# Kernel optimization log

Hardware: AMD Instinct MI355X
Metric: run time of the kernel (lower is better)

Reference implementation:

```python
import jax, jax.numpy as jnp
import numpy as np

IMG = 640.0  # pixel coordinate range for keypoints


def setup_inputs() -> dict:
    key = jax.random.key(0)
    ks = jax.random.split(key, 16)
    B, N, M, C, D, G = 4, 4096, 4096, 256, 256, 32
    s = 1.0 / np.sqrt(C)
    inp = {
        "nodes_t": jax.random.normal(ks[0], (B, N, C), jnp.float32),
        "nodes_t1": jax.random.normal(ks[1], (B, M, C), jnp.float32),
        "kpts_t1_pred": jax.random.uniform(ks[2], (B, N, 2), jnp.float32) * IMG,
        "kpts_t1_actual": jax.random.uniform(ks[3], (B, M, 2), jnp.float32) * IMG,
        "Wq": jax.random.normal(ks[4], (D, C), jnp.float32) * s,
        "bq": jnp.zeros((D,), jnp.float32),
        "Wk": jax.random.normal(ks[5], (D, C), jnp.float32) * s,
        "bk": jnp.zeros((D,), jnp.float32),
        "Wv": jax.random.normal(ks[6], (D, C), jnp.float32) * s,
        "bv": jnp.zeros((D,), jnp.float32),
        "Wm": jax.random.normal(ks[7], (D, D), jnp.float32) * (1.0 / np.sqrt(D)),
        "bm": jnp.zeros((D,), jnp.float32),
        "Wg1": jax.random.normal(ks[8], (G, 3), jnp.float32) * (1.0 / np.sqrt(3.0)),
        "bg1": jnp.zeros((G,), jnp.float32),
        "Wg2": jax.random.normal(ks[9], (G, G), jnp.float32) * (1.0 / np.sqrt(G)),
        "bg2": jnp.zeros((G,), jnp.float32),
        "iter_idx": 0,
    }
    return inp


def reference(nodes_t, nodes_t1, kpts_t1_pred, kpts_t1_actual,
              Wq, bq, Wk, bk, Wv, bv, Wm, bm, Wg1, bg1, Wg2, bg2, iter_idx):
    # window size schedule (iter_idx is a static Python int)
    win = 64.0 if iter_idx == 0 else max(4.0, 32.0 / 2 ** (iter_idx - 1))

    Q = nodes_t @ Wq.T + bq      # [B,N,256]
    K = nodes_t1 @ Wk.T + bk     # [B,M,256]
    V = nodes_t1 @ Wv.T + bv     # [B,M,256]

    # distance-based window mask [B,N,M]
    du = jnp.abs(kpts_t1_pred[:, :, 0:1] - kpts_t1_actual[:, None, :, 0])
    dv = jnp.abs(kpts_t1_pred[:, :, 1:2] - kpts_t1_actual[:, None, :, 1])
    mask = (du < win) & (dv < win)

    attn = jnp.einsum('bnd,bmd->bnm', Q, K) / jnp.sqrt(jnp.float32(256.0))
    attn = jnp.where(mask, attn, jnp.float32(-1e9))
    w = jax.nn.softmax(attn, axis=-1)

    matched_features = jnp.einsum('bnm,bmd->bnd', w, V)        # [B,N,256]
    matched_kpts = jnp.einsum('bnm,bmc->bnc', w, kpts_t1_actual)  # [B,N,2]

    confidence = jnp.any(mask, axis=-1, keepdims=True).astype(jnp.float32)  # [B,N,1]
    flow_residual = (matched_kpts - kpts_t1_pred) * confidence

    geo_in = jnp.concatenate([flow_residual, confidence], axis=-1)  # [B,N,3]
    h = jax.nn.silu(geo_in @ Wg1.T + bg1)
    geo_temp = h @ Wg2.T + bg2                                   # [B,N,32]

    merged = matched_features @ Wm.T + bm                        # [B,N,256]
    return merged, geo_temp, flow_residual, confidence
```

## Files before the change

kernel.cpp:

```cpp
#include <hip/hip_runtime.h>
#include <hip/hip_bf16.h>

typedef unsigned short ushort;
typedef unsigned int uint;
typedef __bf16 bf16x8 __attribute__((ext_vector_type(8)));
typedef float f32x4 __attribute__((ext_vector_type(4)));
typedef ushort ushort8 __attribute__((ext_vector_type(8)));

#define LOG2E 1.4426950408889634f
#define MFMA16(a,b,c) __builtin_amdgcn_mfma_f32_16x16x32_bf16((a),(b),(c),0,0,0)
#define GLL16(src, dst) __builtin_amdgcn_global_load_lds( \
    (const __attribute__((address_space(1))) void*)(src), \
    (__attribute__((address_space(3))) void*)(dst), 16, 0, 0)
#define GLL4(src, dst) __builtin_amdgcn_global_load_lds( \
    (const __attribute__((address_space(1))) void*)(src), \
    (__attribute__((address_space(3))) void*)(dst), 4, 0, 0)

static __device__ __forceinline__ uint packbf(float lo, float hi) {
  union { __bf16 h[2]; uint u; } x;
  x.h[0] = (__bf16)lo; x.h[1] = (__bf16)hi;
  return x.u;
}
static __device__ __forceinline__ int cellof(float x) {
  int c = (int)(x * 0.015625f);
  return c < 0 ? 0 : (c > 9 ? 9 : c);
}

__global__ __launch_bounds__(256) void cast_weights(
    const float* __restrict__ W0, const float* __restrict__ W1,
    const float* __restrict__ W2, const float* __restrict__ W3,
    __bf16* __restrict__ out,
    int* __restrict__ hist, int* __restrict__ curs, float* __restrict__ meanN)
{
  if (blockIdx.x == 0 && blockIdx.y == 0) {
    int t = threadIdx.x;
    for (int i = t; i < 1024; i += 256) { hist[i] = 0; curs[i] = 0; meanN[i] = 0.f; }
  }
  const int which = blockIdx.y;
  const float* src = which == 0 ? W0 : which == 1 ? W1 : which == 2 ? W2 : W3;
  const int i = (blockIdx.x * 256 + threadIdx.x) * 4;
  f32x4 v = *(const f32x4*)(src + i);
  union { __bf16 h[4]; uint u[2]; } x;
  #pragma unroll
  for (int j = 0; j < 4; j++) x.h[j] = (__bf16)v[j];
  *(uint*)(out + (size_t)which * 65536 + i) = x.u[0];
  *(uint*)(out + (size_t)which * 65536 + i + 2) = x.u[1];
}

__global__ __launch_bounds__(256) void hist_kernel(
    const float* __restrict__ kpred, const float* __restrict__ kact,
    int* __restrict__ hist, int* __restrict__ cellpt)
{
  int p = blockIdx.x * 256 + threadIdx.x;
  int type = p >> 14, idx = p & 16383;
  const float2 c = ((const float2*)(type == 0 ? kpred : kact))[idx];
  int cell = cellof(c.x) * 10 + cellof(c.y);
  int b = idx >> 12;
  atomicAdd(&hist[(type * 4 + b) * 128 + cell], 1);
  cellpt[type * 16384 + idx] = cell;
}

__global__ __launch_bounds__(256) void scan_kernel(
    const int* __restrict__ hist, int* __restrict__ strt, int* __restrict__ curs)
{
  __shared__ int sh[1024];
  int t = threadIdx.x;
  for (int i = t; i < 1024; i += 256) sh[i] = hist[i];
  __syncthreads();
  if (t < 8) {
    int run = 0;
    for (int c = 0; c < 100; c++) {
      strt[t * 128 + c] = run;
      curs[t * 128 + c] = run;
      run += sh[t * 128 + c];
    }
    strt[t * 128 + 100] = run;
  }
}

__global__ __launch_bounds__(256) void scatter_kernel(
    const float* __restrict__ kpred, const float* __restrict__ kact,
    const int* __restrict__ cellpt, int* __restrict__ curs,
    int* __restrict__ sq, int* __restrict__ invq, float* __restrict__ kpS,
    int* __restrict__ sk, int* __restrict__ invk, float* __restrict__ kaS)
{
  int p = blockIdx.x * 256 + threadIdx.x;
  int type = p >> 14, idx = p & 16383;
  int b = idx >> 12, n = idx & 4095;
  int cell = cellpt[type * 16384 + idx];
  int pos = atomicAdd(&curs[(type * 4 + b) * 128 + cell], 1);
  if (type == 0) {
    sq[b * 4096 + pos] = n;
    invq[b * 4096 + n] = pos;
    ((float2*)kpS)[b * 4096 + pos] = ((const float2*)kpred)[idx];
  } else {
    sk[b * 4096 + pos] = n;
    invk[b * 4096 + n] = pos;
    ((float2*)kaS)[b * 4096 + pos] = ((const float2*)kact)[idx];
  }
}

__global__ __launch_bounds__(256) void meansum_kernel(
    const float* __restrict__ nodes_t1, float* __restrict__ meanN)
{
  int b = blockIdx.y, chunk = blockIdx.x, c = threadIdx.x;
  const float* base = nodes_t1 + ((size_t)b * 4096 + chunk * 256) * 256 + c;
  float s = 0.f;
  for (int r = 0; r < 256; r++) s += base[(size_t)r * 256];
  atomicAdd(&meanN[b * 256 + c], s);
}

__global__ __launch_bounds__(256) void vmean_kernel(
    const float* __restrict__ meanN, const float* __restrict__ Wv,
    const float* __restrict__ bv, float* __restrict__ Vmean)
{
  __shared__ float mn[256];
  int b = blockIdx.x, d = threadIdx.x;
  mn[d] = meanN[b * 256 + d] * (1.0f / 4096.0f);
  __syncthreads();
  float s = bv[d];
  const float* w = Wv + (size_t)d * 256;
  for (int c = 0; c < 256; c++) s += mn[c] * w[c];
  Vmean[b * 256 + d] = s;
}

__global__ __launch_bounds__(256) void gemm_qkv(
    const float* __restrict__ nodes_t, const float* __restrict__ nodes_t1,
    const ushort* __restrict__ W4,
    const float* __restrict__ bq, const float* __restrict__ bk,
    const float* __restrict__ bv,
    __bf16* __restrict__ outQ, __bf16* __restrict__ outK,
    __bf16* __restrict__ outVs,
    const int* __restrict__ invq, const int* __restrict__ invk)
{
  const int z = blockIdx.z;
  const float* A = z == 0 ? nodes_t : nodes_t1;
  const ushort* W = W4 + z * 65536;
  const float* bias = z == 0 ? bq : (z == 1 ? bk : bv);
  const int* inv = z == 0 ? invq : invk;

  const int wid = threadIdx.x >> 6;
  const int lane = threadIdx.x & 63;
  const int q = lane & 15, g = lane >> 4;
  const int nb = blockIdx.x * 64 + (wid >> 1) * 32;
  const int db = blockIdx.y * 128 + (wid & 1) * 64;

  f32x4 acc[2][4];
  #pragma unroll
  for (int a = 0; a < 2; a++)
    #pragma unroll
    for (int b = 0; b < 4; b++) acc[a][b] = f32x4{0.f,0.f,0.f,0.f};

  const ushort* W0 = W + (size_t)(db + q) * 256 + g * 8;

  #pragma unroll
  for (int c0 = 0; c0 < 256; c0 += 32) {
    bf16x8 a0, a1;
    const float* Ar0 = A + (size_t)(nb + q) * 256 + g * 8 + c0;
    const float* Ar1 = A + (size_t)(nb + 16 + q) * 256 + g * 8 + c0;
    f32x4 u0 = *(const f32x4*)Ar0, u1 = *(const f32x4*)(Ar0 + 4);
    f32x4 w0 = *(const f32x4*)Ar1, w1 = *(const f32x4*)(Ar1 + 4);
    #pragma unroll
    for (int j = 0; j < 4; j++) {
      a0[j] = (__bf16)u0[j]; a0[4 + j] = (__bf16)u1[j];
      a1[j] = (__bf16)w0[j]; a1[4 + j] = (__bf16)w1[j];
    }
    #pragma unroll
    for (int df = 0; df < 4; df++) {
      bf16x8 w = *(const bf16x8*)(W0 + df * 16 * 256 + c0);
      acc[0][df] = MFMA16(a0, w, acc[0][df]);
      acc[1][df] = MFMA16(a1, w, acc[1][df]);
    }
  }
  __bf16* o = z == 0 ? outQ : (z == 1 ? outK : outVs);
  #pragma unroll
  for (int df = 0; df < 4; df++) {
    float bval = bias[db + df * 16 + q];
    #pragma unroll
    for (int nf = 0; nf < 2; nf++)
      #pragma unroll
      for (int r = 0; r < 4; r++) {
        int row = nb + nf * 16 + g * 4 + r;
        int d = db + df * 16 + q;
        float val = acc[nf][df][r] + bval;
        int pos = inv[row];
        o[((size_t)(row & ~4095) + pos) * 256 + d] = (__bf16)val;
      }
  }
}

__global__ __launch_bounds__(256) void transpose_v(
    const ushort* __restrict__ Vs, ushort* __restrict__ VT)
{
  __shared__ ushort tile[64][76];
  const int b = blockIdx.z, rt = blockIdx.x, dt = blockIdx.y;
  const int tid = threadIdx.x;
  const ushort* src = Vs + ((size_t)b * 4096 + rt * 64) * 256 + dt * 64;
  #pragma unroll
  for (int i = 0; i < 2; i++) {
    int c = tid + i * 256;
    int r = c >> 3, dc = (c & 7) * 8;
    ushort8 v = *(const ushort8*)(src + (size_t)r * 256 + dc);
    #pragma unroll
    for (int j = 0; j < 8; j++) tile[r][dc + j] = v[j];
  }
  __syncthreads();
  ushort* dst = VT + ((size_t)b * 256 + dt * 64) * 4096 + rt * 64;
  #pragma unroll
  for (int i = 0; i < 2; i++) {
    int c = tid + i * 256;
    int d = c >> 3, rc = (c & 7) * 8;
    ushort8 v;
    #pragma unroll
    for (int j = 0; j < 8; j++) v[j] = tile[rc + j][d];
    *(ushort8*)(dst + (size_t)d * 4096 + rc) = v;
  }
}

__global__ __launch_bounds__(256) void gemm_merged(
    const ushort* __restrict__ A, const ushort* __restrict__ W,
    const float* __restrict__ bias, float* __restrict__ out)
{
  const int wid = threadIdx.x >> 6;
  const int lane = threadIdx.x & 63;
  const int q = lane & 15, g = lane >> 4;
  const int nb = blockIdx.x * 64 + (wid >> 1) * 32;
  const int db = blockIdx.y * 128 + (wid & 1) * 64;

  f32x4 acc[2][4];
  #pragma unroll
  for (int a = 0; a < 2; a++)
    #pragma unroll
    for (int b = 0; b < 4; b++) acc[a][b] = f32x4{0.f,0.f,0.f,0.f};

  const ushort* W0 = W + (size_t)(db + q) * 256 + g * 8;
  const ushort* Ar0 = A + (size_t)(nb + q) * 256 + g * 8;
  const ushort* Ar1 = A + (size_t)(nb + 16 + q) * 256 + g * 8;

  #pragma unroll
  for (int c0 = 0; c0 < 256; c0 += 32) {
    bf16x8 a0 = *(const bf16x8*)(Ar0 + c0);
    bf16x8 a1 = *(const bf16x8*)(Ar1 + c0);
    #pragma unroll
    for (int df = 0; df < 4; df++) {
      bf16x8 w = *(const bf16x8*)(W0 + df * 16 * 256 + c0);
      acc[0][df] = MFMA16(a0, w, acc[0][df]);
      acc[1][df] = MFMA16(a1, w, acc[1][df]);
    }
  }
  #pragma unroll
  for (int df = 0; df < 4; df++) {
    float bval = bias[db + df * 16 + q];
    #pragma unroll
    for (int nf = 0; nf < 2; nf++)
      #pragma unroll
      for (int r = 0; r < 4; r++) {
        int row = nb + nf * 16 + g * 4 + r;
        out[(size_t)row * 256 + db + df * 16 + q] = acc[nf][df][r] + bval;
      }
  }
}

__global__ __launch_bounds__(256, 2) void attn_kernel(
    const ushort* __restrict__ Q,
    const ushort* __restrict__ K,
    const ushort* __restrict__ VT,
    const float* __restrict__ kpS,
    const int* __restrict__ iter_idx,
    const int* __restrict__ sq,
    const int* __restrict__ strt,
    const float* __restrict__ kaS,
    const float* __restrict__ Vmean,
    __bf16* __restrict__ matched,
    float* __restrict__ out_flow, float* __restrict__ out_conf)
{
  __shared__ __align__(16) ushort Kl[2][8192];
  __shared__ __align__(16) ushort Vl[2][8192];
  __shared__ __align__(16) float2 Cl[2][32];
  __shared__ int tl_t[132], tl_ks[132], tl_ke[132];
  __shared__ int ntile_s;

  const int tid = threadIdx.x;
  const int wid = tid >> 6, lane = tid & 63;
  const int q = lane & 15, g = lane >> 4;
  const int batch = blockIdx.x & 3;
  const int cell = blockIdx.x >> 2;

  const int qstart = strt[batch * 128 + cell];
  const int nq = strt[batch * 128 + cell + 1] - qstart;
  if (nq == 0) return;

  const int cu = cell / 10, cv = cell % 10;
  const int c0 = cv > 0 ? cv - 1 : 0, c1 = cv < 9 ? cv + 1 : 9;
  const int* kst = strt + (4 + batch) * 128;

  if (tid == 0) {
    int n = 0;
    int lo = cu > 0 ? cu - 1 : 0, hi = cu < 9 ? cu + 1 : 9;
    for (int cc = lo; cc <= hi; cc++) {
      int ks = kst[cc * 10 + c0];
      int ke = kst[cc * 10 + c1 + 1];
      for (int t = ks & ~31; t < ke; t += 32) {
        tl_t[n] = t; tl_ks[n] = ks; tl_ke[n] = ke; n++;
      }
    }
    ntile_s = n;
  }
  __syncthreads();
  const int ntile = ntile_s;

  const int idx = *iter_idx;
  const float win = (idx == 0) ? 64.0f : fmaxf(4.0f, ldexpf(32.0f, 1 - idx));

  const ushort* Kbase = K + (size_t)batch * 4096 * 256;
  const ushort* VTb = VT + (size_t)batch * 1048576;
  const float* kasf = kaS + (size_t)batch * 8192;
  const float* Vm = Vmean + batch * 256;

  const int npass = (nq + 63) >> 6;

  auto STAGE = [&](int ti, int b) {
    const int t = tl_t[ti];
    #pragma unroll
    for (int j = 0; j < 4; j++) {
      int n = wid * 256 + j * 64 + lane;
      int r = n & 31, u = n >> 5;
      GLL16(Kbase + (size_t)(t + r) * 256 + u * 8,
            &Kl[b][(size_t)(wid * 256 + j * 64) * 8]);
    }
    #pragma unroll
    for (int j = 0; j < 4; j++) {
      int n = wid * 256 + j * 64 + lane;
      int pl = n >> 8, d = n & 255;
      GLL16(VTb + (size_t)d * 4096 + t + pl * 8,
            &Vl[b][(size_t)(wid * 256 + j * 64) * 8]);
    }
    if (wid == 0) GLL4(kasf + t * 2 + lane, &Cl[b][0]);
  };

  int cnt = 0, qi = 0;
  bool active = false;
  float pu = 0.f, pv = 0.f;
  bf16x8 qf[8];
  f32x4 O[16];
  float m_run = -1e9f, l_run = 0.f, u_run = 0.f, v_run = 0.f;

  auto PASS_INIT = [&](int pp) {
    int tbase = pp * 64 + wid * 16;
    active = tbase < nq;
    cnt = active ? min(16, nq - tbase) : 0;
    if (active) {
      int qq = q < cnt ? q : cnt - 1;
      int qsrow = batch * 4096 + qstart + tbase + qq;
      qi = sq[qsrow];
      const ushort* qptr = Q + (size_t)qsrow * 256 + g * 8;
      #pragma unroll
      for (int mf = 0; mf < 8; mf++) qf[mf] = *(const bf16x8*)(qptr + mf * 32);
      float2 kpv = ((const float2*)kpS)[qsrow];
      pu = kpv.x; pv = kpv.y;
    }
    #pragma unroll
    for (int i = 0; i < 16; i++) O[i] = f32x4{0.f,0.f,0.f,0.f};
    m_run = -1e9f; l_run = 0.f; u_run = 0.f; v_run = 0.f;
  };

  auto EPILOGUE = [&]() {
    if (!active) return;
    l_run += __shfl_xor(l_run, 16); l_run += __shfl_xor(l_run, 32);
    u_run += __shfl_xor(u_run, 16); u_run += __shfl_xor(u_run, 32);
    v_run += __shfl_xor(v_run, 16); v_run += __shfl_xor(v_run, 32);
    bool degen = (m_run <= -5e8f) || (l_run == 0.f);
    float rinv = degen ? 0.f : 1.0f / l_run;
    if (g == 0 && q < cnt) {
      float conf = degen ? 0.f : 1.0f;
      int row = batch * 4096 + qi;
      float fu = (u_run * rinv - pu) * conf, fv = (v_run * rinv - pv) * conf;
      ((float2*)out_flow)[row] = float2{fu, fv};
      out_conf[row] = conf;
    }
    #pragma unroll
    for (int r = 0; r < 4; r++) {
      int src = 4 * g + r;
      int qi_r = __shfl(qi, src);
      float il_r = __shfl(rinv, src);
      bool dg_r = (il_r == 0.f);
      if (src < cnt) {
        __bf16* mrow = matched + ((size_t)batch * 4096 + qi_r) * 256;
        #pragma unroll
        for (int df = 0; df < 16; df++) {
          float val = dg_r ? Vm[df * 16 + q] : O[df][r] * il_r;
          mrow[df * 16 + q] = (__bf16)val;
        }
      }
    }
  };

  if (ntile == 0) {
    for (int pp = 0; pp < npass; pp++) { PASS_INIT(pp); EPILOGUE(); }
    return;
  }

  const int total = npass * ntile;
  STAGE(0, 0);
  PASS_INIT(0);

  int i = 0, pp = 0;
  for (int it = 0; it < total; ++it) {
    __syncthreads();
    if (it + 1 < total) {
      int ni = (i + 1 == ntile) ? 0 : i + 1;
      STAGE(ni, (it + 1) & 1);
    }
    const int b = it & 1;

    if (active) {
      const int t = tl_t[i], ks = tl_ks[i], ke = tl_ke[i];

      f32x4 s0a = {0.f,0.f,0.f,0.f}, s0b = {0.f,0.f,0.f,0.f};
      f32x4 s1a = {0.f,0.f,0.f,0.f}, s1b = {0.f,0.f,0.f,0.f};
      #pragma unroll
      for (int mf = 0; mf < 8; mf += 2) {
        bf16x8 ka0 = *(const bf16x8*)&Kl[b][(size_t)(((mf    ) * 4 + g) * 32 + q     ) * 8];
        bf16x8 kb0 = *(const bf16x8*)&Kl[b][(size_t)(((mf + 1) * 4 + g) * 32 + q     ) * 8];
        bf16x8 ka1 = *(const bf16x8*)&Kl[b][(size_t)(((mf    ) * 4 + g) * 32 + q + 16) * 8];
        bf16x8 kb1 = *(const bf16x8*)&Kl[b][(size_t)(((mf + 1) * 4 + g) * 32 + q + 16) * 8];
        s0a = MFMA16(ka0, qf[mf],     s0a);
        s0b = MFMA16(kb0, qf[mf + 1], s0b);
        s1a = MFMA16(ka1, qf[mf],     s1a);
        s1b = MFMA16(kb1, qf[mf + 1], s1b);
      }

      float aus[8], avs[8], sv[8];
      #pragma unroll
      for (int r = 0; r < 4; r++) {
        int jr = t + 4 * g + r;
        float2 cc0 = Cl[b][4 * g + r];
        aus[r] = cc0.x; avs[r] = cc0.y;
        bool val = (jr >= ks && jr < ke);
        float du = fabsf(pu - cc0.x), dv = fabsf(pv - cc0.y);
        float sr = s0a[r] + s0b[r];
        sv[r] = (val && fmaxf(du, dv) < win) ? sr * 0.0625f : -1e9f;

        int jr1 = jr + 16;
        float2 cc1 = Cl[b][16 + 4 * g + r];
        aus[4 + r] = cc1.x; avs[4 + r] = cc1.y;
        val = (jr1 >= ks && jr1 < ke);
        du = fabsf(pu - cc1.x); dv = fabsf(pv - cc1.y);
        sr = s1a[r] + s1b[r];
        sv[4 + r] = (val && fmaxf(du, dv) < win) ? sr * 0.0625f : -1e9f;
      }

      float mt = fmaxf(fmaxf(fmaxf(sv[0], sv[1]), fmaxf(sv[2], sv[3])),
                       fmaxf(fmaxf(sv[4], sv[5]), fmaxf(sv[6], sv[7])));
      mt = fmaxf(mt, __shfl_xor(mt, 16));
      mt = fmaxf(mt, __shfl_xor(mt, 32));
      if (__any(mt > m_run + 8.0f)) {
        float m_new = fmaxf(m_run, mt);
        float scale = exp2f((m_run - m_new) * LOG2E);
        l_run *= scale; u_run *= scale; v_run *= scale;
        float s_r[4];
        #pragma unroll
        for (int r = 0; r < 4; r++) s_r[r] = __shfl(scale, 4 * g + r);
        #pragma unroll
        for (int df = 0; df < 16; df++)
          #pragma unroll
          for (int r = 0; r < 4; r++) O[df][r] *= s_r[r];
        m_run = m_new;
      }

      float p[8];
      #pragma unroll
      for (int ii = 0; ii < 8; ii++) p[ii] = exp2f((sv[ii] - m_run) * LOG2E);
      #pragma unroll
      for (int ii = 0; ii < 8; ii++) {
        l_run += p[ii];
        u_run += p[ii] * aus[ii];
        v_run += p[ii] * avs[ii];
      }

      uint d0 = packbf(p[0], p[1]), d1 = packbf(p[2], p[3]);
      uint d2 = packbf(p[4], p[5]), d3 = packbf(p[6], p[7]);
      int srcA = q + ((g & 1) << 5);
      int srcB = srcA + 16;
      uint x0 = (uint)__shfl((int)d0, srcA), x1 = (uint)__shfl((int)d1, srcA);
      uint x2 = (uint)__shfl((int)d0, srcB), x3 = (uint)__shfl((int)d1, srcB);
      uint y0 = (uint)__shfl((int)d2, srcA), y1 = (uint)__shfl((int)d3, srcA);
      uint y2 = (uint)__shfl((int)d2, srcB), y3 = (uint)__shfl((int)d3, srcB);
      union { uint i4[4]; bf16x8 v; } af;
      bool lo = (g < 2);
      af.i4[0] = lo ? x0 : y0; af.i4[1] = lo ? x1 : y1;
      af.i4[2] = lo ? x2 : y2; af.i4[3] = lo ? x3 : y3;

      #pragma unroll
      for (int df = 0; df < 16; df++) {
        bf16x8 vfd = *(const bf16x8*)&Vl[b][(size_t)(g * 256 + df * 16 + q) * 8];
        O[df] = MFMA16(af.v, vfd, O[df]);
      }
    }

    if (i == ntile - 1) {
      EPILOGUE();
      pp++;
      if (pp < npass) PASS_INIT(pp);
      i = 0;
    } else {
      i++;
    }
  }
}

__global__ __launch_bounds__(256) void geo_kernel(
    const float* __restrict__ flow, const float* __restrict__ conf_in,
    const float* __restrict__ Wg1, const float* __restrict__ bg1,
    const float* __restrict__ Wg2, const float* __restrict__ bg2,
    float* __restrict__ out_geo)
{
  __shared__ float w1[32][3], b1[32], b2[32];
  __shared__ __align__(16) float w2[32][32];
  int tid = threadIdx.x;
  for (int i = tid; i < 96; i += 256) w1[i / 3][i % 3] = Wg1[i];
  if (tid < 32) { b1[tid] = bg1[tid]; b2[tid] = bg2[tid]; }
  for (int i = tid; i < 1024; i += 256) w2[i / 32][i % 32] = Wg2[i];
  __syncthreads();

  int row = blockIdx.x * 256 + tid;
  float2 f = ((const float2*)flow)[row];
  float c = conf_in[row];
  float h[32];
  #pragma unroll
  for (int j = 0; j < 32; j++) {
    float x = w1[j][0] * f.x + w1[j][1] * f.y + w1[j][2] * c + b1[j];
    h[j] = x / (1.f + __expf(-x));
  }
  #pragma unroll
  for (int o = 0; o < 32; o += 2) {
    float s0 = b2[o], s1 = b2[o + 1];
    #pragma unroll
    for (int j = 0; j < 32; j += 4) {
      f32x4 wa = *(const f32x4*)&w2[o][j];
      f32x4 wb = *(const f32x4*)&w2[o + 1][j];
      s0 += wa[0]*h[j] + wa[1]*h[j+1] + wa[2]*h[j+2] + wa[3]*h[j+3];
      s1 += wb[0]*h[j] + wb[1]*h[j+1] + wb[2]*h[j+2] + wb[3]*h[j+3];
    }
    ((float2*)out_geo)[((size_t)row * 32 + o) >> 1] = float2{s0, s1};
  }
}

extern "C" void kernel_launch(void* const* d_in, const int* in_sizes, int n_in,
                              void* d_out, int out_size, void* d_ws, size_t ws_size,
                              hipStream_t stream) {
  const float* nodes_t  = (const float*)d_in[0];
  const float* nodes_t1 = (const float*)d_in[1];
  const float* kpred    = (const float*)d_in[2];
  const float* kact     = (const float*)d_in[3];
  const float* Wq = (const float*)d_in[4];  const float* bq = (const float*)d_in[5];
  const float* Wk = (const float*)d_in[6];  const float* bk = (const float*)d_in[7];
  const float* Wv = (const float*)d_in[8];  const float* bv = (const float*)d_in[9];
  const float* Wm = (const float*)d_in[10]; const float* bm = (const float*)d_in[11];
  const float* Wg1= (const float*)d_in[12]; const float* bg1= (const float*)d_in[13];
  const float* Wg2= (const float*)d_in[14]; const float* bg2= (const float*)d_in[15];
  const int* iter = (const int*)d_in[16];

  float* out_merged = (float*)d_out;
  float* out_geo  = out_merged + 4 * 4096 * 256;
  float* out_flow = out_geo + 4 * 4096 * 32;
  float* out_conf = out_flow + 4 * 4096 * 2;

  ushort* wsQ   = (ushort*)d_ws;
  ushort* wsK   = wsQ + 4194304;
  ushort* wsVT  = wsK + 4194304;
  ushort* wsM   = wsVT + 4194304;
  ushort* wsW   = wsM + 4194304;
  float*  kaS   = (float*)(wsW + 262144);
  float*  kpS   = kaS + 32768;
  float*  meanN = kpS + 32768;
  float*  Vmean = meanN + 1024;
  int*    hist  = (int*)(Vmean + 1024);
  int*    strt  = hist + 1024;
  int*    curs  = strt + 1024;
  int*    cellpt= curs + 1024;
  int*    sq    = cellpt + 32768;
  int*    sk    = sq + 16384;
  int*    invk  = sk + 16384;
  int*    invq  = invk + 16384;

  dim3 cg(64, 4, 1);
  cast_weights<<<cg, 256, 0, stream>>>(Wq, Wk, Wv, Wm, (__bf16*)wsW,
                                       hist, curs, meanN);
  hist_kernel<<<128, 256, 0, stream>>>(kpred, kact, hist, cellpt);
  scan_kernel<<<1, 256, 0, stream>>>(hist, strt, curs);
  scatter_kernel<<<128, 256, 0, stream>>>(kpred, kact, cellpt, curs,
                                          sq, invq, kpS, sk, invk, kaS);
  dim3 mg(16, 4, 1);
  meansum_kernel<<<mg, 256, 0, stream>>>(nodes_t1, meanN);
  vmean_kernel<<<4, 256, 0, stream>>>(meanN, Wv, bv, Vmean);

  dim3 qg(256, 2, 3);
  gemm_qkv<<<qg, 256, 0, stream>>>(nodes_t, nodes_t1, wsW, bq, bk, bv,
                                   (__bf16*)wsQ, (__bf16*)wsK, (__bf16*)wsM,
                                   invq, invk);
  dim3 tg(64, 4, 4);
  transpose_v<<<tg, 256, 0, stream>>>(wsM, wsVT);
  attn_kernel<<<400, 256, 0, stream>>>(wsQ, wsK, wsVT, kpS, iter,
                                       sq, strt, kaS, Vmean,
                                       (__bf16*)wsM, out_flow, out_conf);
  dim3 gg(256, 2, 1);
  gemm_merged<<<gg, 256, 0, stream>>>(wsM, wsW + 196608, bm, out_merged);
  geo_kernel<<<64, 256, 0, stream>>>(out_flow, out_conf, Wg1, bg1, Wg2, bg2, out_geo);
}
```

Measured before the change: 213.1 us.

## Stage K/V tiles through registers with XOR-swizzled LDS layout instead of direct global-to-LDS loads

Replaces the direct global_load_lds staging of K and V^T tiles with coalesced global loads into registers, issued before compute and written to LDS after compute for the next buffer. The K tile layout in LDS is XOR-swizzled to reduce bank conflicts on the MFMA operand reads. The barrier moves to the end of each iteration. Each thread now holds eight more uint4 registers, which may lower occupancy, and the LDS write happens after compute instead of overlapping with it asynchronously.

Result: slower. 259.6 us (median of 2 runs) (+21.8%).

```diff
diff --git a/kernel.cpp b/kernel.cpp
--- a/kernel.cpp
+++ b/kernel.cpp
@@ -9,9 +9,6 @@
 
 #define LOG2E 1.4426950408889634f
 #define MFMA16(a,b,c) __builtin_amdgcn_mfma_f32_16x16x32_bf16((a),(b),(c),0,0,0)
-#define GLL16(src, dst) __builtin_amdgcn_global_load_lds( \
-    (const __attribute__((address_space(1))) void*)(src), \
-    (__attribute__((address_space(3))) void*)(dst), 16, 0, 0)
 #define GLL4(src, dst) __builtin_amdgcn_global_load_lds( \
     (const __attribute__((address_space(1))) void*)(src), \
     (__attribute__((address_space(3))) void*)(dst), 4, 0, 0)
@@ -319,23 +316,35 @@
 
   const int npass = (nq + 63) >> 6;
 
-  auto STAGE = [&](int ti, int b) {
+  uint4 kreg[4], vreg[4];
+
+  auto STAGE_LOAD = [&](int ti, int buf) {
     const int t = tl_t[ti];
     #pragma unroll
     for (int j = 0; j < 4; j++) {
-      int n = wid * 256 + j * 64 + lane;
-      int r = n & 31, u = n >> 5;
-      GLL16(Kbase + (size_t)(t + r) * 256 + u * 8,
-            &Kl[b][(size_t)(wid * 256 + j * 64) * 8]);
+      int r = wid * 8 + j * 2 + (lane >> 5);
+      kreg[j] = *(const uint4*)(Kbase + (size_t)(t + r) * 256 + (lane & 31) * 8);
     }
     #pragma unroll
     for (int j = 0; j < 4; j++) {
-      int n = wid * 256 + j * 64 + lane;
-      int pl = n >> 8, d = n & 255;
-      GLL16(VTb + (size_t)d * 4096 + t + pl * 8,
-            &Vl[b][(size_t)(wid * 256 + j * 64) * 8]);
-    }
-    if (wid == 0) GLL4(kasf + t * 2 + lane, &Cl[b][0]);
+      int d = wid * 64 + j * 16 + (lane >> 2);
+      vreg[j] = *(const uint4*)(VTb + (size_t)d * 4096 + t + (lane & 3) * 8);
+    }
+    if (wid == 0) GLL4(kasf + t * 2 + lane, &Cl[buf][0]);
+  };
+
+  auto STAGE_WRITE = [&](int buf) {
+    #pragma unroll
+    for (int j = 0; j < 4; j++) {
+      int r = wid * 8 + j * 2 + (lane >> 5);
+      int u = lane & 31;
+      *(uint4*)&Kl[buf][(u * 32 + (r ^ (u & 7))) * 8] = kreg[j];
+    }
+    #pragma unroll
+    for (int j = 0; j < 4; j++) {
+      int d = wid * 64 + j * 16 + (lane >> 2);
+      *(uint4*)&Vl[buf][((lane & 3) * 256 + d) * 8] = vreg[j];
+    }
   };
 
   int cnt = 0, qi = 0;
@@ -401,17 +410,18 @@
   }
 
   const int total = npass * ntile;
-  STAGE(0, 0);
+  STAGE_LOAD(0, 0);
+  STAGE_WRITE(0);
   PASS_INIT(0);
+  __syncthreads();
 
   int i = 0, pp = 0;
   for (int it = 0; it < total; ++it) {
-    __syncthreads();
-    if (it + 1 < total) {
-      int ni = (i + 1 == ntile) ? 0 : i + 1;
-      STAGE(ni, (it + 1) & 1);
-    }
     const int b = it & 1;
+    const bool more = (it + 1 < total);
+    const int ni = (i + 1 == ntile) ? 0 : i + 1;
+
+    if (more) STAGE_LOAD(ni, (it + 1) & 1);
 
     if (active) {
       const int t = tl_t[i], ks = tl_ks[i], ke = tl_ke[i];
@@ -420,10 +430,11 @@
       f32x4 s1a = {0.f,0.f,0.f,0.f}, s1b = {0.f,0.f,0.f,0.f};
       #pragma unroll
       for (int mf = 0; mf < 8; mf += 2) {
-        bf16x8 ka0 = *(const bf16x8*)&Kl[b][(size_t)(((mf    ) * 4 + g) * 32 + q     ) * 8];
-        bf16x8 kb0 = *(const bf16x8*)&Kl[b][(size_t)(((mf + 1) * 4 + g) * 32 + q     ) * 8];
-        bf16x8 ka1 = *(const bf16x8*)&Kl[b][(size_t)(((mf    ) * 4 + g) * 32 + q + 16) * 8];
-        bf16x8 kb1 = *(const bf16x8*)&Kl[b][(size_t)(((mf + 1) * 4 + g) * 32 + q + 16) * 8];
+        const int u0 = mf * 4 + g, u1 = (mf + 1) * 4 + g;
+        bf16x8 ka0 = *(const bf16x8*)&Kl[b][(u0 * 32 + ((q     ) ^ (u0 & 7))) * 8];
+        bf16x8 kb0 = *(const bf16x8*)&Kl[b][(u1 * 32 + ((q     ) ^ (u1 & 7))) * 8];
+        bf16x8 ka1 = *(const bf16x8*)&Kl[b][(u0 * 32 + ((q + 16) ^ (u0 & 7))) * 8];
+        bf16x8 kb1 = *(const bf16x8*)&Kl[b][(u1 * 32 + ((q + 16) ^ (u1 & 7))) * 8];
         s0a = MFMA16(ka0, qf[mf],     s0a);
         s0b = MFMA16(kb0, qf[mf + 1], s0b);
         s1a = MFMA16(ka1, qf[mf],     s1a);
@@ -498,6 +509,8 @@
       }
     }
 
+    if (more) STAGE_WRITE((it + 1) & 1);
+
     if (i == ntile - 1) {
       EPILOGUE();
       pp++;
@@ -506,6 +519,7 @@
     } else {
       i++;
     }
+    __syncthreads();
   }
 }
 
```
